# Performance work log

Hardware: AMD Instinct MI355X
Metric: run time of the kernel (lower is better)

## Reference

```python
import jax, jax.numpy as jnp
import numpy as np


def setup_inputs() -> dict:
    key = jax.random.key(0)
    k1, k2 = jax.random.split(key)
    B, N, M = 4, 16384, 4096
    src_points = jax.random.normal(k1, (B, N, 3), dtype=jnp.float32)
    target_verts = jax.random.normal(k2, (B, M, 3), dtype=jnp.float32)
    return {"src_points": src_points, "target_verts": target_verts}


def reference(src_points, target_verts):
    # target_faces=None path of ChamferLoss: degenerate one-vertex triangles,
    # so closest-point-on-mesh == nearest target vertex.
    # d2[b,n,m] = ||p_bn - v_bm||^2 via the expansion p2 + v2 - 2 p.v
    p2 = jnp.sum(src_points * src_points, axis=-1)          # (B, N)
    v2 = jnp.sum(target_verts * target_verts, axis=-1)      # (B, M)
    pv = jnp.einsum('bnd,bmd->bnm', src_points, target_verts)  # (B, N, M)
    d2 = p2[:, :, None] + v2[:, None, :] - 2.0 * pv
    d2 = jnp.maximum(d2, 0.0)
    min_d2 = jnp.min(d2, axis=-1)                            # (B, N)
    num_src_per_batch = src_points.shape[1]
    loss = jnp.sum(min_d2, axis=-1) / num_src_per_batch      # (B,)
    return loss
```

## Files before the change

### kernel.cpp

```cpp
#include <hip/hip_runtime.h>
#include <float.h>


typedef __bf16 bf16x8 __attribute__((ext_vector_type(8)));
typedef float  f32x16 __attribute__((ext_vector_type(16)));

constexpr int B = 4, N = 16384, M = 4096;
constexpr int BN = B * N;
constexpr int NCHUNK = 4;
constexpr int CHUNK_V = M / NCHUNK;
constexpr int TILES = CHUNK_V / 32;
constexpr int TPB = 256;
constexpr int PPB = 256;
constexpr int PBLK = BN / PPB;
constexpr size_t BFRAG_BYTES = (size_t)B * M * 32;

__global__ __launch_bounds__(256) void chamfer_pre(
    const float* __restrict__ tv, unsigned char* __restrict__ bfr,
    float* __restrict__ out)
{
    if (blockIdx.x == 0 && threadIdx.x < B) out[threadIdx.x] = 0.0f;
    int i = blockIdx.x * 256 + threadIdx.x;
    int b = i >> 12;
    int m = i & (M - 1);
    float x = tv[3 * i + 0], y = tv[3 * i + 1], z = tv[3 * i + 2];
    __bf16 xh = (__bf16)x, yh = (__bf16)y, zh = (__bf16)z;
    float xhf = (float)xh, yhf = (float)yh, zhf = (float)zh;
    __bf16 xl = (__bf16)(x - xhf), yl = (__bf16)(y - yhf), zl = (__bf16)(z - zhf);
    float v2 = fmaf(x, x, fmaf(y, y, z * z));
    __bf16 v2h = (__bf16)v2;
    __bf16 v2l = (__bf16)(v2 - (float)v2h);
    __bf16 zero = (__bf16)0.0f;

    bf16x8 h0, h1;
    h0[0] = (__bf16)(-2.0f * xhf); h0[1] = (__bf16)(-2.0f * yhf);
    h0[2] = (__bf16)(-2.0f * zhf);
    h0[3] = h0[0]; h0[4] = h0[1]; h0[5] = h0[2];
    h0[6] = (__bf16)(-2.0f * (float)xl); h0[7] = (__bf16)(-2.0f * (float)yl);
    h1[0] = (__bf16)(-2.0f * (float)zl); h1[1] = v2h; h1[2] = v2l;
    h1[3] = zero; h1[4] = zero; h1[5] = zero; h1[6] = zero; h1[7] = zero;

    int chunk = m >> 10, local = m & (CHUNK_V - 1), tile = local >> 5, c = m & 31;
    size_t base = (size_t)b * 131072 + (size_t)chunk * 32768 + tile * 1024 + c * 16;
    *(bf16x8*)(bfr + base)       = h0;
    *(bf16x8*)(bfr + base + 512) = h1;
}

__global__ __launch_bounds__(TPB) void chamfer_mfma(
    const float* __restrict__ src, const unsigned char* __restrict__ bfr,
    float* __restrict__ partial)
{
    __shared__ float epi[4 * 2 * 32 * 33];
    const int blk   = blockIdx.x;
    const int chunk = blk & 3;
    const int pblk  = blk >> 2;
    const int b     = pblk >> 6;
    const int t     = threadIdx.x;
    const int w     = t >> 6, L = t & 63;
    const int half  = L >> 5, c = L & 31;

    const int gpa = pblk * 256 + w * 64 + c;
    const int gpb = gpa + 32;
    float ax = src[3*gpa], ay = src[3*gpa+1], az = src[3*gpa+2];
    float bx = src[3*gpb], by = src[3*gpb+1], bz = src[3*gpb+2];
    __bf16 one = (__bf16)1.0f, zero = (__bf16)0.0f;
    bf16x8 aA, aB;
    {
        __bf16 xh=(__bf16)ax, yh=(__bf16)ay, zh=(__bf16)az;
        __bf16 xl=(__bf16)(ax-(float)xh), yl=(__bf16)(ay-(float)yh), zl=(__bf16)(az-(float)zh);
        if (half == 0) { aA[0]=xh; aA[1]=yh; aA[2]=zh; aA[3]=xl; aA[4]=yl; aA[5]=zl; aA[6]=xh; aA[7]=yh; }
        else { aA[0]=zh; aA[1]=one; aA[2]=one; aA[3]=zero; aA[4]=zero; aA[5]=zero; aA[6]=zero; aA[7]=zero; }
    }
    {
        __bf16 xh=(__bf16)bx, yh=(__bf16)by, zh=(__bf16)bz;
        __bf16 xl=(__bf16)(bx-(float)xh), yl=(__bf16)(by-(float)yh), zl=(__bf16)(bz-(float)zh);
        if (half == 0) { aB[0]=xh; aB[1]=yh; aB[2]=zh; aB[3]=xl; aB[4]=yl; aB[5]=zl; aB[6]=xh; aB[7]=yh; }
        else { aB[0]=zh; aB[1]=one; aB[2]=one; aB[3]=zero; aB[4]=zero; aB[5]=zero; aB[6]=zero; aB[7]=zero; }
    }

    f32x16 mnA, mnB, zeroC;
#pragma unroll
    for (int r = 0; r < 16; ++r) { mnA[r] = FLT_MAX; mnB[r] = FLT_MAX; zeroC[r] = 0.0f; }

    const char* bp = (const char*)bfr + (size_t)b * 131072
                   + (size_t)chunk * 32768 + half * 512 + c * 16;
#pragma unroll 4
    for (int tl = 0; tl < TILES; ++tl) {
        bf16x8 bf = *(const bf16x8*)(bp + (size_t)tl * 1024);
        f32x16 Ca = __builtin_amdgcn_mfma_f32_32x32x16_bf16(aA, bf, zeroC, 0, 0, 0);
        f32x16 Cb = __builtin_amdgcn_mfma_f32_32x32x16_bf16(aB, bf, zeroC, 0, 0, 0);
#pragma unroll
        for (int r = 0; r < 16; ++r) {
            mnA[r] = fminf(mnA[r], Ca[r]);
            mnB[r] = fminf(mnB[r], Cb[r]);
        }
    }

    float* epw = epi + w * (2 * 32 * 33);
#pragma unroll
    for (int r = 0; r < 16; ++r) {
        int row = (r & 3) + 8 * (r >> 2) + 4 * half;
        epw[row * 33 + c]        = mnA[r];
        epw[(32 + row) * 33 + c] = mnB[r];
    }
    __syncthreads();

    const float* myrow = epi + w * (2 * 32 * 33) + (L >> 5) * (32 * 33) + (L & 31) * 33;
    float m = myrow[0];
#pragma unroll
    for (int k = 1; k < 32; ++k) m = fminf(m, myrow[k]);
    partial[(size_t)chunk * BN + pblk * 256 + w * 64 + L] = m;
}

__global__ __launch_bounds__(256) void chamfer_reduce(
    const float* __restrict__ partial, const float* __restrict__ src,
    float* __restrict__ out)
{
    const int p = blockIdx.x * 256 + threadIdx.x;
    const int b = blockIdx.x >> 6;
    float m = fminf(fminf(partial[p], partial[(size_t)BN + p]),
                    fminf(partial[2 * (size_t)BN + p], partial[3 * (size_t)BN + p]));
    float x = src[3*p], y = src[3*p+1], z = src[3*p+2];
    float pp = fmaf(x, x, fmaf(y, y, z * z));
    float sum = fmaxf(m + pp, 0.0f);

    for (int off = 32; off > 0; off >>= 1)
        sum += __shfl_down(sum, off, 64);
    __shared__ float acc[4];
    if ((threadIdx.x & 63) == 0) acc[threadIdx.x >> 6] = sum;
    __syncthreads();
    if (threadIdx.x == 0) {
        float s = acc[0] + acc[1] + acc[2] + acc[3];
        atomicAdd(&out[b], s * (1.0f / N));
    }
}

extern "C" void kernel_launch(void* const* d_in, const int* in_sizes, int n_in,
                              void* d_out, int out_size, void* d_ws, size_t ws_size,
                              hipStream_t stream) {
    const float* src = (const float*)d_in[0];
    const float* tv  = (const float*)d_in[1];
    float* out = (float*)d_out;
    unsigned char* bfr = (unsigned char*)d_ws;
    float* partial = (float*)((char*)d_ws + BFRAG_BYTES);

    chamfer_pre   <<<(B * M) / 256, 256, 0, stream>>>(tv, bfr, out);
    chamfer_mfma  <<<PBLK * NCHUNK, TPB, 0, stream>>>(src, bfr, partial);
    chamfer_reduce<<<BN / 256, 256, 0, stream>>>(partial, src, out);
}
```

Measured before the change: 76.05 us.

## Stage vertex fragments in LDS, halve points per block, shuffle-reduce epilogue

Each block now copies its 32KB chunk of precomputed bf16 vertex fragments into LDS and runs the MFMA loop from LDS, instead of reading them from global memory on every tile. Points per block drop from 256 to 128, so each wave runs one MFMA chain instead of two. A launch-bounds occupancy hint is added to keep more blocks resident. The epilogue's LDS transpose and barrier are replaced by xor-shuffle min reductions across the 32 columns. The risk is less instruction-level parallelism per wave and an extra LDS fill per block, traded against more blocks and lower global-load latency.

```diff
diff --git a/kernel.cpp b/kernel.cpp
--- a/kernel.cpp
+++ b/kernel.cpp
@@ -11,7 +11,7 @@
 constexpr int CHUNK_V = M / NCHUNK;
 constexpr int TILES = CHUNK_V / 32;
 constexpr int TPB = 256;
-constexpr int PPB = 256;
+constexpr int PPB = 128;
 constexpr int PBLK = BN / PPB;
 constexpr size_t BFRAG_BYTES = (size_t)B * M * 32;
 
@@ -46,70 +46,62 @@
     *(bf16x8*)(bfr + base + 512) = h1;
 }
 
-__global__ __launch_bounds__(TPB) void chamfer_mfma(
+__global__ __launch_bounds__(TPB, 4) void chamfer_mfma(
     const float* __restrict__ src, const unsigned char* __restrict__ bfr,
     float* __restrict__ partial)
 {
-    __shared__ float epi[4 * 2 * 32 * 33];
+    __shared__ uint4 lds4[2048];
+    const char* ldsc = (const char*)lds4;
     const int blk   = blockIdx.x;
     const int chunk = blk & 3;
     const int pblk  = blk >> 2;
-    const int b     = pblk >> 6;
+    const int b     = pblk >> 7;
     const int t     = threadIdx.x;
     const int w     = t >> 6, L = t & 63;
     const int half  = L >> 5, c = L & 31;
 
-    const int gpa = pblk * 256 + w * 64 + c;
-    const int gpb = gpa + 32;
-    float ax = src[3*gpa], ay = src[3*gpa+1], az = src[3*gpa+2];
-    float bx = src[3*gpb], by = src[3*gpb+1], bz = src[3*gpb+2];
+    const uint4* gsrc = (const uint4*)(bfr + (size_t)b * 131072 + (size_t)chunk * 32768);
+#pragma unroll
+    for (int i = 0; i < 8; ++i) lds4[i * 256 + t] = gsrc[i * 256 + t];
+
+    const int gp = pblk * PPB + w * 32 + c;
+    float ax = src[3*gp], ay = src[3*gp+1], az = src[3*gp+2];
     __bf16 one = (__bf16)1.0f, zero = (__bf16)0.0f;
-    bf16x8 aA, aB;
+    bf16x8 aA;
     {
         __bf16 xh=(__bf16)ax, yh=(__bf16)ay, zh=(__bf16)az;
         __bf16 xl=(__bf16)(ax-(float)xh), yl=(__bf16)(ay-(float)yh), zl=(__bf16)(az-(float)zh);
         if (half == 0) { aA[0]=xh; aA[1]=yh; aA[2]=zh; aA[3]=xl; aA[4]=yl; aA[5]=zl; aA[6]=xh; aA[7]=yh; }
         else { aA[0]=zh; aA[1]=one; aA[2]=one; aA[3]=zero; aA[4]=zero; aA[5]=zero; aA[6]=zero; aA[7]=zero; }
     }
-    {
-        __bf16 xh=(__bf16)bx, yh=(__bf16)by, zh=(__bf16)bz;
-        __bf16 xl=(__bf16)(bx-(float)xh), yl=(__bf16)(by-(float)yh), zl=(__bf16)(bz-(float)zh);
-        if (half == 0) { aB[0]=xh; aB[1]=yh; aB[2]=zh; aB[3]=xl; aB[4]=yl; aB[5]=zl; aB[6]=xh; aB[7]=yh; }
-        else { aB[0]=zh; aB[1]=one; aB[2]=one; aB[3]=zero; aB[4]=zero; aB[5]=zero; aB[6]=zero; aB[7]=zero; }
+
+    f32x16 mn, zeroC;
+#pragma unroll
+    for (int r = 0; r < 16; ++r) { mn[r] = FLT_MAX; zeroC[r] = 0.0f; }
+
+    __syncthreads();
+
+    const int laneoff = half * 512 + c * 16;
+#pragma unroll 4
+    for (int tl = 0; tl < TILES; ++tl) {
+        bf16x8 bf = *(const bf16x8*)(ldsc + tl * 1024 + laneoff);
+        f32x16 C = __builtin_amdgcn_mfma_f32_32x32x16_bf16(aA, bf, zeroC, 0, 0, 0);
+#pragma unroll
+        for (int r = 0; r < 16; ++r) mn[r] = fminf(mn[r], C[r]);
     }
 
-    f32x16 mnA, mnB, zeroC;
 #pragma unroll
-    for (int r = 0; r < 16; ++r) { mnA[r] = FLT_MAX; mnB[r] = FLT_MAX; zeroC[r] = 0.0f; }
-
-    const char* bp = (const char*)bfr + (size_t)b * 131072
-                   + (size_t)chunk * 32768 + half * 512 + c * 16;
-#pragma unroll 4
-    for (int tl = 0; tl < TILES; ++tl) {
-        bf16x8 bf = *(const bf16x8*)(bp + (size_t)tl * 1024);
-        f32x16 Ca = __builtin_amdgcn_mfma_f32_32x32x16_bf16(aA, bf, zeroC, 0, 0, 0);
-        f32x16 Cb = __builtin_amdgcn_mfma_f32_32x32x16_bf16(aB, bf, zeroC, 0, 0, 0);
+    for (int off = 16; off > 0; off >>= 1) {
 #pragma unroll
-        for (int r = 0; r < 16; ++r) {
-            mnA[r] = fminf(mnA[r], Ca[r]);
-            mnB[r] = fminf(mnB[r], Cb[r]);
-        }
+        for (int r = 0; r < 16; ++r)
+            mn[r] = fminf(mn[r], __shfl_xor(mn[r], off, 64));
     }
-
-    float* epw = epi + w * (2 * 32 * 33);
+    float* pout = partial + (size_t)chunk * BN + pblk * PPB + w * 32;
 #pragma unroll
     for (int r = 0; r < 16; ++r) {
         int row = (r & 3) + 8 * (r >> 2) + 4 * half;
-        epw[row * 33 + c]        = mnA[r];
-        epw[(32 + row) * 33 + c] = mnB[r];
+        if (c == row) pout[row] = mn[r];
     }
-    __syncthreads();
-
-    const float* myrow = epi + w * (2 * 32 * 33) + (L >> 5) * (32 * 33) + (L & 31) * 33;
-    float m = myrow[0];
-#pragma unroll
-    for (int k = 1; k < 32; ++k) m = fminf(m, myrow[k]);
-    partial[(size_t)chunk * BN + pblk * 256 + w * 64 + L] = m;
 }
 
 __global__ __launch_bounds__(256) void chamfer_reduce(
```

Result: no change. 77.04 us (+1.3%).
